# Performance work log

Measured on AMD Instinct MI355X. Metric: run time of the kernel, lower is better.

The kernel has to match this reference:

```python
import jax, jax.numpy as jnp
import numpy as np

NODE_DIM = 64
EDGE_DIM = 64
HIDDEN = 128
B, N = 2, 512

def setup_inputs() -> dict:
    key = jax.random.key(0)
    ks = jax.random.split(key, 8)
    node_feature = jax.random.normal(ks[0], (B, N, NODE_DIM), dtype=jnp.float32)
    adjacency = (jax.random.uniform(ks[1], (B, N, N)) < 0.1).astype(jnp.float32)
    target_information = jax.random.normal(ks[2], (B, N, NODE_DIM), dtype=jnp.float32)
    edge_feature = jax.random.normal(ks[3], (B, N, N, EDGE_DIM), dtype=jnp.float32)
    node_mask = jnp.ones((B, N), dtype=jnp.float32)
    # edge_fc: Dense(2*node_dim + edge_dim -> hidden) + ReLU
    W_edge = jax.random.normal(ks[4], (2 * NODE_DIM + EDGE_DIM, HIDDEN), dtype=jnp.float32) * 0.05
    b_edge = jnp.zeros((HIDDEN,), dtype=jnp.float32)
    # feature_fc: Dense(hidden + node_dim -> hidden) + ReLU
    W_feat = jax.random.normal(ks[5], (HIDDEN + NODE_DIM, HIDDEN), dtype=jnp.float32) * 0.05
    b_feat = jnp.zeros((HIDDEN,), dtype=jnp.float32)
    return {"node_feature": node_feature, "adjacency": adjacency,
            "target_information": target_information, "edge_feature": edge_feature,
            "node_mask": node_mask, "W_edge": W_edge, "b_edge": b_edge,
            "W_feat": W_feat, "b_feat": b_feat}

def reference(node_feature, adjacency, target_information, edge_feature, node_mask,
              W_edge, b_edge, W_feat, b_feat):
    D = node_feature.shape[-1]
    # concat([node_i, node_j, edge]) @ W_edge == node_i@W1 + node_j@W2 + edge@W3
    # (avoids materializing the [B,N,N,2D+E] concat tensor)
    W1, W2, W3 = W_edge[:D], W_edge[D:2 * D], W_edge[2 * D:]
    hi = jnp.einsum('bnd,dh->bnh', node_feature, W1)   # contribution of node i (rows)
    hj = jnp.einsum('bnd,dh->bnh', node_feature, W2)   # contribution of node j (cols)
    he = jnp.einsum('bije,eh->bijh', edge_feature, W3)  # [B,N,N,H]
    edge_h = jax.nn.relu(hi[:, :, None, :] + hj[:, None, :, :] + he + b_edge)
    # masked sum over neighbors j -> message [B,N,H]
    message = jnp.einsum('bijh,bij->bih', edge_h, adjacency)
    # feature_fc on concat([message, node_feature])
    H = message.shape[-1]
    ending = jax.nn.relu(jnp.einsum('bnh,hk->bnk', message, W_feat[:H])
                         + jnp.einsum('bnd,dk->bnk', node_feature, W_feat[H:])
                         + b_feat)
    return (ending, edge_h, target_information)
```

## Files before the change

### kernel.cpp

```cpp
#include <hip/hip_runtime.h>
#include <hip/hip_bf16.h>

#define NB 2
#define NN 512
#define ND 64
#define NH 128

typedef __attribute__((ext_vector_type(8))) short short8;
typedef __attribute__((ext_vector_type(4))) float f32x4;

__device__ __forceinline__ short f2s(float x) {
    __hip_bfloat16 h = __float2bfloat16(x);
    return *reinterpret_cast<short*>(&h);
}

__device__ __forceinline__ short8 cvt8(const float* p) {
    f32x4 a = *(const f32x4*)p;
    f32x4 b = *(const f32x4*)(p + 4);
    short8 r;
    r[0] = f2s(a[0]); r[1] = f2s(a[1]); r[2] = f2s(a[2]); r[3] = f2s(a[3]);
    r[4] = f2s(b[0]); r[5] = f2s(b[1]); r[6] = f2s(b[2]); r[7] = f2s(b[3]);
    return r;
}

__global__ __launch_bounds__(128) void bias_kernel(
    const float* __restrict__ node,
    const float* __restrict__ W_edge,
    const float* __restrict__ b_edge,
    float* __restrict__ bias)
{
    int bn = blockIdx.x;
    int h = threadIdx.x;
    __shared__ float nrow[ND];
    if (h < ND) nrow[h] = node[bn * ND + h];
    __syncthreads();
    float acc = b_edge[h];
    #pragma unroll
    for (int d = 0; d < ND; d++)
        acc += nrow[d] * W_edge[d * NH + h];
    bias[bn * NH + h] = acc;
}

__global__ __launch_bounds__(256) void edge_kernel(
    const float* __restrict__ ef,
    const float* __restrict__ node,
    const float* __restrict__ adj,
    const float* __restrict__ W_edge,
    const float* __restrict__ bias,
    float* __restrict__ edge_out,
    float* __restrict__ message)
{
    constexpr int BTS = NH + 8;
    __shared__ short BT[NH * BTS];
    __shared__ float msgbuf[4][NH];

    int blk = blockIdx.x;
    int b = blk >> 9;
    int tid = threadIdx.x;

    for (int t = tid; t < NH * NH; t += 256) {
        int h = t >> 7;
        int k = t & 127;
        int row = (k < ND) ? (2 * ND + k) : k;
        BT[h * BTS + k] = f2s(W_edge[row * NH + h]);
    }
    __syncthreads();

    int lane = tid & 63;
    int wave = tid >> 6;
    int m = lane & 15;
    int quad = lane >> 4;

    float bias_l[8];
    #pragma unroll
    for (int ht = 0; ht < 8; ht++)
        bias_l[ht] = bias[blk * NH + ht * 16 + m];

    float msg_l[8] = {0.f, 0.f, 0.f, 0.f, 0.f, 0.f, 0.f, 0.f};

    const float* adjrow = adj + (size_t)blk * NN;
    float* outbase = edge_out + (size_t)blk * NN * NH;

    for (int c = 0; c < 8; c++) {
        int j0 = wave * 128 + c * 16;
        int jm = j0 + m;
        const float* efp = ef + ((size_t)blk * NN + jm) * ND;
        const float* ndp = node + ((size_t)b * NN + jm) * ND;
        short8 af[4];
        af[0] = cvt8(efp + quad * 8);
        af[1] = cvt8(efp + 32 + quad * 8);
        af[2] = cvt8(ndp + quad * 8);
        af[3] = cvt8(ndp + 32 + quad * 8);

        float av[4];
        #pragma unroll
        for (int r = 0; r < 4; r++)
            av[r] = adjrow[j0 + quad * 4 + r];

        #pragma unroll
        for (int ht = 0; ht < 8; ht++) {
            f32x4 acc = {0.f, 0.f, 0.f, 0.f};
            const short* bt = BT + (ht * 16 + m) * BTS;
            #pragma unroll
            for (int kf = 0; kf < 4; kf++) {
                short8 bfr = *(const short8*)(bt + kf * 32 + quad * 8);
                acc = __builtin_amdgcn_mfma_f32_16x16x32_bf16(af[kf], bfr, acc, 0, 0, 0);
            }
            int h = ht * 16 + m;
            float bsum = bias_l[ht];
            #pragma unroll
            for (int r = 0; r < 4; r++) {
                float v = acc[r] + bsum;
                v = fmaxf(v, 0.f);
                int j = j0 + quad * 4 + r;
                outbase[(size_t)j * NH + h] = v;
                msg_l[ht] += av[r] * v;
            }
        }
    }

    #pragma unroll
    for (int ht = 0; ht < 8; ht++) {
        float v = msg_l[ht];
        v += __shfl_xor(v, 16, 64);
        v += __shfl_xor(v, 32, 64);
        if (quad == 0) msgbuf[wave][ht * 16 + m] = v;
    }
    __syncthreads();
    if (tid < NH) {
        float s = msgbuf[0][tid] + msgbuf[1][tid] + msgbuf[2][tid] + msgbuf[3][tid];
        message[(size_t)blk * NH + tid] = s;
    }
}

__global__ __launch_bounds__(128) void out_kernel(
    const float* __restrict__ node,
    const float* __restrict__ message,
    const float* __restrict__ W_feat,
    const float* __restrict__ b_feat,
    float* __restrict__ ending)
{
    int bn = blockIdx.x;
    int k = threadIdx.x;
    __shared__ float mrow[NH];
    __shared__ float nrow[ND];
    mrow[k] = message[(size_t)bn * NH + k];
    if (k < ND) nrow[k] = node[bn * ND + k];
    __syncthreads();
    float acc = b_feat[k];
    #pragma unroll 4
    for (int h = 0; h < NH; h++)
        acc += mrow[h] * W_feat[h * NH + k];
    #pragma unroll 4
    for (int d = 0; d < ND; d++)
        acc += nrow[d] * W_feat[(NH + d) * NH + k];
    ending[(size_t)bn * NH + k] = fmaxf(acc, 0.f);
}

extern "C" void kernel_launch(void* const* d_in, const int* in_sizes, int n_in,
                              void* d_out, int out_size, void* d_ws, size_t ws_size,
                              hipStream_t stream)
{
    const float* node   = (const float*)d_in[0];
    const float* adj    = (const float*)d_in[1];
    const float* tgt    = (const float*)d_in[2];
    const float* ef     = (const float*)d_in[3];
    const float* W_edge = (const float*)d_in[5];
    const float* b_edge = (const float*)d_in[6];
    const float* W_feat = (const float*)d_in[7];
    const float* b_feat = (const float*)d_in[8];

    float* out_ending = (float*)d_out;
    float* out_edge   = out_ending + (size_t)NB * NN * NH;
    float* out_tgt    = out_edge + (size_t)NB * NN * NN * NH;

    float* bias    = (float*)d_ws;
    float* message = bias + (size_t)NB * NN * NH;

    bias_kernel<<<NB * NN, NH, 0, stream>>>(node, W_edge, b_edge, bias);
    edge_kernel<<<NB * NN, 256, 0, stream>>>(ef, node, adj, W_edge, bias, out_edge, message);
    out_kernel<<<NB * NN, NH, 0, stream>>>(node, message, W_feat, b_feat, out_ending);
    hipMemcpyAsync(out_tgt, tgt, (size_t)NB * NN * ND * sizeof(float),
                   hipMemcpyDeviceToDevice, stream);
}
```

Measured before the change: 442.9 us.

## Fuse bias, edge and output kernels; transpose MFMA for vectorized edge stores

Merges the three kernels into one: each block computes its node's edge bias at the start and, after the message reduction, computes the feature_fc output itself. This drops two launches and the workspace round trips for bias and message. The MFMA operands are swapped so each lane holds four consecutive hidden values, which allows 16-byte stores of edge_h. The bias is loaded as the accumulator's initial value, and the message reduction now uses shuffles across the row lanes. The W_edge transpose into LDS changes its index order, which may alter LDS bank-conflict behavior.

```diff
diff --git a/kernel.cpp b/kernel.cpp
--- a/kernel.cpp
+++ b/kernel.cpp
@@ -5,6 +5,7 @@
 #define NN 512
 #define ND 64
 #define NH 128
+#define BTS (NH + 8)
 
 typedef __attribute__((ext_vector_type(8))) short short8;
 typedef __attribute__((ext_vector_type(4))) float f32x4;
@@ -23,67 +24,61 @@
     return r;
 }
 
-__global__ __launch_bounds__(128) void bias_kernel(
-    const float* __restrict__ node,
-    const float* __restrict__ W_edge,
-    const float* __restrict__ b_edge,
-    float* __restrict__ bias)
-{
-    int bn = blockIdx.x;
-    int h = threadIdx.x;
-    __shared__ float nrow[ND];
-    if (h < ND) nrow[h] = node[bn * ND + h];
-    __syncthreads();
-    float acc = b_edge[h];
-    #pragma unroll
-    for (int d = 0; d < ND; d++)
-        acc += nrow[d] * W_edge[d * NH + h];
-    bias[bn * NH + h] = acc;
-}
-
-__global__ __launch_bounds__(256) void edge_kernel(
+__global__ __launch_bounds__(256) void fused_kernel(
     const float* __restrict__ ef,
     const float* __restrict__ node,
     const float* __restrict__ adj,
     const float* __restrict__ W_edge,
-    const float* __restrict__ bias,
+    const float* __restrict__ b_edge,
+    const float* __restrict__ W_feat,
+    const float* __restrict__ b_feat,
     float* __restrict__ edge_out,
-    float* __restrict__ message)
+    float* __restrict__ ending)
 {
-    constexpr int BTS = NH + 8;
     __shared__ short BT[NH * BTS];
+    __shared__ float nrow_s[ND];
+    __shared__ float bias_s[NH];
+    __shared__ float red_s[NH];
     __shared__ float msgbuf[4][NH];
+    __shared__ float msg_s[NH];
 
     int blk = blockIdx.x;
     int b = blk >> 9;
     int tid = threadIdx.x;
 
     for (int t = tid; t < NH * NH; t += 256) {
-        int h = t >> 7;
-        int k = t & 127;
+        int k = t >> 7;
+        int h = t & 127;
         int row = (k < ND) ? (2 * ND + k) : k;
         BT[h * BTS + k] = f2s(W_edge[row * NH + h]);
     }
+    if (tid < ND) nrow_s[tid] = node[(size_t)blk * ND + tid];
     __syncthreads();
 
-    int lane = tid & 63;
-    int wave = tid >> 6;
-    int m = lane & 15;
-    int quad = lane >> 4;
+    {
+        int h = tid & 127, half = tid >> 7;
+        float acc = 0.f;
+        #pragma unroll
+        for (int d = half * 32; d < half * 32 + 32; d++)
+            acc += nrow_s[d] * W_edge[d * NH + h];
+        if (half) red_s[h] = acc;
+        __syncthreads();
+        if (!half) bias_s[h] = acc + red_s[h] + b_edge[h];
+        __syncthreads();
+    }
 
-    float bias_l[8];
+    int lane = tid & 63, wave = tid >> 6;
+    int m = lane & 15, quad = lane >> 4;
+
+    float msg_l[32];
     #pragma unroll
-    for (int ht = 0; ht < 8; ht++)
-        bias_l[ht] = bias[blk * NH + ht * 16 + m];
-
-    float msg_l[8] = {0.f, 0.f, 0.f, 0.f, 0.f, 0.f, 0.f, 0.f};
+    for (int t = 0; t < 32; t++) msg_l[t] = 0.f;
 
     const float* adjrow = adj + (size_t)blk * NN;
     float* outbase = edge_out + (size_t)blk * NN * NH;
 
     for (int c = 0; c < 8; c++) {
-        int j0 = wave * 128 + c * 16;
-        int jm = j0 + m;
+        int jm = wave * 128 + c * 16 + m;
         const float* efp = ef + ((size_t)blk * NN + jm) * ND;
         const float* ndp = node + ((size_t)b * NN + jm) * ND;
         short8 af[4];
@@ -91,70 +86,62 @@
         af[1] = cvt8(efp + 32 + quad * 8);
         af[2] = cvt8(ndp + quad * 8);
         af[3] = cvt8(ndp + 32 + quad * 8);
+        float adjv = adjrow[jm];
 
-        float av[4];
-        #pragma unroll
-        for (int r = 0; r < 4; r++)
-            av[r] = adjrow[j0 + quad * 4 + r];
-
+        float* outrow = outbase + (size_t)jm * NH;
         #pragma unroll
         for (int ht = 0; ht < 8; ht++) {
-            f32x4 acc = {0.f, 0.f, 0.f, 0.f};
+            f32x4 acc = *(const f32x4*)(bias_s + ht * 16 + quad * 4);
             const short* bt = BT + (ht * 16 + m) * BTS;
             #pragma unroll
             for (int kf = 0; kf < 4; kf++) {
                 short8 bfr = *(const short8*)(bt + kf * 32 + quad * 8);
-                acc = __builtin_amdgcn_mfma_f32_16x16x32_bf16(af[kf], bfr, acc, 0, 0, 0);
+                acc = __builtin_amdgcn_mfma_f32_16x16x32_bf16(bfr, af[kf], acc, 0, 0, 0);
             }
-            int h = ht * 16 + m;
-            float bsum = bias_l[ht];
+            f32x4 v;
             #pragma unroll
             for (int r = 0; r < 4; r++) {
-                float v = acc[r] + bsum;
-                v = fmaxf(v, 0.f);
-                int j = j0 + quad * 4 + r;
-                outbase[(size_t)j * NH + h] = v;
-                msg_l[ht] += av[r] * v;
+                v[r] = fmaxf(acc[r], 0.f);
+                msg_l[ht * 4 + r] += adjv * v[r];
             }
+            *(f32x4*)(outrow + ht * 16 + quad * 4) = v;
         }
     }
 
     #pragma unroll
-    for (int ht = 0; ht < 8; ht++) {
-        float v = msg_l[ht];
-        v += __shfl_xor(v, 16, 64);
-        v += __shfl_xor(v, 32, 64);
-        if (quad == 0) msgbuf[wave][ht * 16 + m] = v;
+    for (int t = 0; t < 32; t++) {
+        float v = msg_l[t];
+        v += __shfl_xor(v, 1, 64);
+        v += __shfl_xor(v, 2, 64);
+        v += __shfl_xor(v, 4, 64);
+        v += __shfl_xor(v, 8, 64);
+        msg_l[t] = v;
+    }
+    if (m == 0) {
+        #pragma unroll
+        for (int ht = 0; ht < 8; ht++)
+            #pragma unroll
+            for (int r = 0; r < 4; r++)
+                msgbuf[wave][ht * 16 + quad * 4 + r] = msg_l[ht * 4 + r];
     }
     __syncthreads();
-    if (tid < NH) {
-        float s = msgbuf[0][tid] + msgbuf[1][tid] + msgbuf[2][tid] + msgbuf[3][tid];
-        message[(size_t)blk * NH + tid] = s;
+    if (tid < NH)
+        msg_s[tid] = msgbuf[0][tid] + msgbuf[1][tid] + msgbuf[2][tid] + msgbuf[3][tid];
+    __syncthreads();
+
+    {
+        int k = tid & 127, half = tid >> 7;
+        float acc = 0.f;
+        #pragma unroll 4
+        for (int hh = half * 64; hh < half * 64 + 64; hh++)
+            acc += msg_s[hh] * W_feat[hh * NH + k];
+        #pragma unroll 4
+        for (int d = half * 32; d < half * 32 + 32; d++)
+            acc += nrow_s[d] * W_feat[(NH + d) * NH + k];
+        if (half) red_s[k] = acc;
+        __syncthreads();
+        if (!half) ending[(size_t)blk * NH + k] = fmaxf(acc + red_s[k] + b_feat[k], 0.f);
     }
-}
-
-__global__ __launch_bounds__(128) void out_kernel(
-    const float* __restrict__ node,
-    const float* __restrict__ message,
-    const float* __restrict__ W_feat,
-    const float* __restrict__ b_feat,
-    float* __restrict__ ending)
-{
-    int bn = blockIdx.x;
-    int k = threadIdx.x;
-    __shared__ float mrow[NH];
-    __shared__ float nrow[ND];
-    mrow[k] = message[(size_t)bn * NH + k];
-    if (k < ND) nrow[k] = node[bn * ND + k];
-    __syncthreads();
-    float acc = b_feat[k];
-    #pragma unroll 4
-    for (int h = 0; h < NH; h++)
-        acc += mrow[h] * W_feat[h * NH + k];
-    #pragma unroll 4
-    for (int d = 0; d < ND; d++)
-        acc += nrow[d] * W_feat[(NH + d) * NH + k];
-    ending[(size_t)bn * NH + k] = fmaxf(acc, 0.f);
 }
 
 extern "C" void kernel_launch(void* const* d_in, const int* in_sizes, int n_in,
@@ -174,12 +161,8 @@
     float* out_edge   = out_ending + (size_t)NB * NN * NH;
     float* out_tgt    = out_edge + (size_t)NB * NN * NN * NH;
 
-    float* bias    = (float*)d_ws;
-    float* message = bias + (size_t)NB * NN * NH;
-
-    bias_kernel<<<NB * NN, NH, 0, stream>>>(node, W_edge, b_edge, bias);
-    edge_kernel<<<NB * NN, 256, 0, stream>>>(ef, node, adj, W_edge, bias, out_edge, message);
-    out_kernel<<<NB * NN, NH, 0, stream>>>(node, message, W_feat, b_feat, out_ending);
+    fused_kernel<<<NB * NN, 256, 0, stream>>>(ef, node, adj, W_edge, b_edge,
+                                              W_feat, b_feat, out_edge, out_ending);
     hipMemcpyAsync(out_tgt, tgt, (size_t)NB * NN * ND * sizeof(float),
                    hipMemcpyDeviceToDevice, stream);
 }
```

After: 415.6 us (median of 2 runs). 1.07x faster.
